# Optimization experiments

Measured on AMD Instinct MI355X. Metric: run time of the kernel, lower is better.

## Reference

```python
import jax, jax.numpy as jnp
import numpy as np

UNITS = 32      # 12 inter + 19 command + 1 motor
SENSORY = 32    # dense_2 output dim
MOTOR = 1
ODE_UNFOLDS = 6
EPS = 1e-8


def _build_wiring():
    # kerasncp NCP wiring: motor ids [0,1), command [1,20), inter [20,32)
    rng = np.random.RandomState(42)
    inter = np.arange(20, 32)
    command = np.arange(1, 20)
    motor = np.arange(0, 1)
    adj = np.zeros((UNITS, UNITS), np.float32)
    sens = np.zeros((SENSORY, UNITS), np.float32)
    for s in range(SENSORY):                      # sensory_fanout=6 onto inter neurons
        for d in rng.choice(inter, 6, replace=False):
            sens[s, d] = rng.choice([-1.0, 1.0])
    for i in inter:                               # inter_fanout=4 onto command neurons
        for d in rng.choice(command, 4, replace=False):
            adj[i, d] = rng.choice([-1.0, 1.0])
    for _ in range(6):                            # 6 recurrent command synapses
        adj[rng.choice(command), rng.choice(command)] = rng.choice([-1.0, 1.0])
    for m in motor:                               # motor_fanin=4 from command neurons
        for srcn in rng.choice(command, 4, replace=False):
            adj[srcn, m] = rng.choice([-1.0, 1.0])
    return adj, sens


def setup_inputs() -> dict:
    key = jax.random.key(0)
    ks = jax.random.split(key, 12)
    B, T = 256, 1024
    adj, sens = _build_wiring()
    u = lambda k, sh, lo, hi: jax.random.uniform(k, sh, jnp.float32, lo, hi)
    return {
        "x": jax.random.normal(ks[0], (B, T, 2), jnp.float32),
        "d1_w": jax.random.normal(ks[1], (2, 128), jnp.float32) * (1.0 / np.sqrt(2.0)),
        "d1_b": jnp.zeros((128,), jnp.float32),
        "d2_w": jax.random.normal(ks[2], (128, SENSORY), jnp.float32) * (1.0 / np.sqrt(128.0)),
        "d2_b": jnp.zeros((SENSORY,), jnp.float32),
        "input_w": jnp.ones((SENSORY,), jnp.float32),
        "input_b": jnp.zeros((SENSORY,), jnp.float32),
        "output_w": jnp.ones((MOTOR,), jnp.float32),
        "output_b": jnp.zeros((MOTOR,), jnp.float32),
        "gleak": u(ks[3], (UNITS,), 0.001, 1.0),
        "vleak": u(ks[4], (UNITS,), -0.2, 0.2),
        "cm": u(ks[5], (UNITS,), 0.4, 0.6),
        "w_syn": u(ks[6], (UNITS, UNITS), 0.001, 1.0),
        "mu": u(ks[7], (UNITS, UNITS), 0.3, 0.8),
        "sigma": u(ks[8], (UNITS, UNITS), 3.0, 8.0),
        "erev": jnp.asarray(adj),
        "sensory_w": u(ks[9], (SENSORY, UNITS), 0.001, 1.0),
        "sensory_mu": u(ks[10], (SENSORY, UNITS), 0.3, 0.8),
        "sensory_sigma": u(ks[11], (SENSORY, UNITS), 3.0, 8.0),
        "sensory_erev": jnp.asarray(sens),
        "sparsity_mask": jnp.asarray(np.abs(adj), jnp.int32),
        "sensory_mask": jnp.asarray(np.abs(sens), jnp.int32),
    }


def reference(x, d1_w, d1_b, d2_w, d2_b, input_w, input_b, output_w, output_b,
              gleak, vleak, cm, w_syn, mu, sigma, erev,
              sensory_w, sensory_mu, sensory_sigma, sensory_erev,
              sparsity_mask, sensory_mask):
    # Dense stack (per timestep)
    h = jax.nn.relu(x @ d1_w + d1_b)          # [B,T,128]
    h = h @ d2_w + d2_b                        # [B,T,32] sensory inputs
    spm = sparsity_mask.astype(h.dtype)
    ssm = sensory_mask.astype(h.dtype)

    def gate(v, m, s):                         # v [B,pre] -> [B,pre,post]
        return jax.nn.sigmoid(s * (v[..., None] - m))

    cm_t = cm * ODE_UNFOLDS                    # cm / (elapsed_time / ode_unfolds), elapsed_time=1

    def step(v, xt):
        inp = xt * input_w + input_b           # LTC input mapping (affine)
        sa = sensory_w * gate(inp, sensory_mu, sensory_sigma) * ssm   # [B,32,32]
        wnum_s = jnp.sum(sa * sensory_erev, axis=1)                   # [B,32]
        wden_s = jnp.sum(sa, axis=1)

        def unfold(vp, _):
            wa = w_syn * gate(vp, mu, sigma) * spm                    # [B,32,32]
            wnum = jnp.sum(wa * erev, axis=1) + wnum_s
            wden = jnp.sum(wa, axis=1) + wden_s
            vp = (cm_t * vp + gleak * vleak + wnum) / (cm_t + gleak + wden + EPS)
            return vp, None

        v, _ = jax.lax.scan(unfold, v, None, length=ODE_UNFOLDS)
        return v, None

    v0 = jnp.zeros((h.shape[0], UNITS), h.dtype)
    vT, _ = jax.lax.scan(step, v0, jnp.swapaxes(h, 0, 1))  # scan over T
    # output mapping: motor neurons are the first MOTOR states
    return vT[:, :MOTOR] * output_w + output_b             # [B,1]
```

## Files before the change

kernel.cpp:

```cpp
#include <hip/hip_runtime.h>
#include <math.h>

#define NB 256
#define NT 1024
#define NUNF 6
#define TBS 128
#define CHK 8
#define NTJMAX 12
#define L2E 1.44269504088896340736f
#define PI_F 3.14159265358979324f

typedef const float* fp;

extern "C" __device__ float __ocml_exp2_f32(float);
__device__ __forceinline__ float frcp(float x) { return __builtin_amdgcn_rcpf(x); }
__device__ __forceinline__ float ex2(float x) { return __ocml_exp2_f32(x); }
__device__ __forceinline__ float sgm(float a, float b, float v) { return frcp(1.f + ex2(fmaf(a, v, b))); }

struct Tables {
    int ngroups, npos, nchunks, ntraj;
    int grp_start[21];
    int ord[20];
    int pos[20];
    int aff[20];
    int need_traj[20];
    int traj_slot[20];
    int ch_ps[20], ch_pe[20], ch_gs[20], ch_ge[20];
    int ncp[20], nip[20], ngp[20];
    float cmt[20], cn0[20], cd0[20];
    float icmt[12];
    int   cp_pre[20][8];
    float cp_a[20][8], cp_b[20][8], cp_w[20][8], cp_e[20][8];
    int   ip_i[20][12];
    float ip_a[20][12], ip_b[20][12], ip_w[20][12], ip_e[20][12];
    int   gp_pre[20][6];
    float gp_a[20][6], gp_b[20][6], gp_w[20][6], gp_e[20][6];
};

struct DenseTab {
    int cnt[12];
    float in0[12], id0[12];
    int   pre[12][32];
    float a[12][32], b[12][32], w[12][32], e[12][32];
    int homog, maxcnt;
};

#define WS_DTAB   16384
#define WS_BND    24576
#define WS_BMASK  25600
#define WS_MG     32768
#define WS_VST    98304
#define WS_SENSI  131072

__global__ void build_tables(fp wsyn, fp mu, fp sigma, fp erev, const int* spm,
                             fp sw, fp smu, fp ssg, fp serev, const int* smask,
                             fp cm, fp gleak, fp vleak, fp d1b, Tables* T, DenseTab* D) {
    __shared__ int   spmL[1024], smkL[1024];
    __shared__ float wL[1024], muL[1024], sgL[1024], evL[1024];
    __shared__ float swL[1024], smuL[1024], ssgL[1024], sevL[1024];
    __shared__ float cmL[32], glL[32], vlL[32];
    __shared__ int premaskL[20], ancL[20], rootL[20], depUL[20], keyL[20], posL[20], ordL[20];
    __shared__ int ngpL[20], ntjL[20], slotU[20];
    __shared__ int neededS;
    __shared__ float habs[64];
    __shared__ int cntS[12];
    int tid = threadIdx.x;
    for (int k = tid; k < 1024; k += 64) {
        spmL[k] = spm[k]; wL[k] = wsyn[k]; muL[k] = mu[k]; sgL[k] = sigma[k]; evL[k] = erev[k];
        smkL[k] = smask[k]; swL[k] = sw[k]; smuL[k] = smu[k]; ssgL[k] = ssg[k]; sevL[k] = serev[k];
    }
    if (tid < 32) { cmL[tid] = cm[tid]; glL[tid] = gleak[tid]; vlL[tid] = vleak[tid]; }
    habs[tid] = fmaxf(fabsf(d1b[tid]), fabsf(d1b[tid + 64]));
    __syncthreads();
    if (tid < 20) {
        int pm = 0;
        for (int i = 0; i < 20; ++i) if (spmL[i * 32 + tid]) pm |= 1 << i;
        premaskL[tid] = pm;
        ancL[tid] = pm;
    }
    __syncthreads();
    for (int it = 0; it < 20; ++it) {
        int a = 0;
        if (tid < 20) {
            a = ancL[tid];
            int pm = premaskL[tid];
            for (int i = 0; i < 20; ++i) if ((pm >> i) & 1) a |= ancL[i];
        }
        __syncthreads();
        if (tid < 20) ancL[tid] = a;
        __syncthreads();
    }
    if (tid == 0) neededS = ancL[0] | 1;
    __syncthreads();
    int needed = neededS;
    if (tid < 20) {
        int r = tid;
        if ((needed >> tid) & 1) {
            int aj = ancL[tid];
            for (int i = 0; i < 20; ++i)
                if (i < r && ((needed >> i) & 1) && ((aj >> i) & 1) && ((ancL[i] >> tid) & 1)) r = i;
        }
        rootL[tid] = r;
        depUL[tid] = 0;
    }
    __syncthreads();
    for (int it = 0; it < 21; ++it) {
        int d = 0;
        if (tid < 20 && ((needed >> tid) & 1)) {
            int pm = premaskL[tid], myr = rootL[tid];
            for (int i = 0; i < 20; ++i)
                if (((pm >> i) & 1) && rootL[i] != myr) d = max(d, depUL[i] + 1);
        }
        __syncthreads();
        if (tid < 20 && d > depUL[tid]) depUL[tid] = d;
        __syncthreads();
    }
    if (tid < 20) {
        int key = 0x7FFFFFFF;
        if ((needed >> tid) & 1) {
            int myr = rootL[tid], dg = 0;
            for (int i = 0; i < 20; ++i)
                if (((needed >> i) & 1) && rootL[i] == myr) dg = max(dg, depUL[i]);
            key = dg * 32 + myr;
        }
        keyL[tid] = key;
    }
    __syncthreads();
    if (tid < 20) {
        int mykey = keyL[tid];
        int p = 0;
        for (int k = 0; k < 20; ++k)
            if (keyL[k] < mykey || (keyL[k] == mykey && k < tid)) ++p;
        posL[tid] = p;
        if (p < 20) ordL[p] = tid;
    }
    __syncthreads();
    if (tid < 20) {
        int nt = 0;
        if ((needed >> tid) & 1)
            for (int j = 0; j < 20; ++j)
                if (j != tid && ((needed >> j) & 1) && spmL[tid * 32 + j]) { nt = 1; break; }
        ntjL[tid] = nt;
    }
    __syncthreads();
    if (tid == 0) {
        int s = 0;
        for (int p = 0; p < 20; ++p) { int u = ordL[p]; slotU[u] = s; s += ntjL[u]; }
        T->ntraj = s;
    }
    __syncthreads();
    if (tid < 20) {
        int j = tid, cc = 0, ci = 0, cg = 0;
        T->cmt[j] = cmL[j] * (float)NUNF;
        T->cn0[j] = glL[j] * vlL[j];
        T->cd0[j] = cmL[j] * (float)NUNF + glL[j] + 1e-8f;
        if ((needed >> j) & 1) {
            int myr = rootL[j];
            int mystart = posL[myr];
            for (int i = 0; i < 32; ++i) {
                int p = i * 32 + j;
                if (!spmL[p]) continue;
                float sg = sgL[p];
                float a = -sg * L2E, b = sg * muL[p] * L2E;
                float w = wL[p], e = w * evL[p];
                if (i >= 20) {
                    T->ip_i[j][ci] = i - 20;
                    T->ip_a[j][ci] = a; T->ip_b[j][ci] = b; T->ip_w[j][ci] = w; T->ip_e[j][ci] = e;
                    ++ci;
                } else if (rootL[i] == myr) {
                    T->gp_pre[j][cg] = posL[i] - mystart;
                    T->gp_a[j][cg] = a; T->gp_b[j][cg] = b; T->gp_w[j][cg] = w; T->gp_e[j][cg] = e;
                    ++cg;
                } else {
                    T->cp_pre[j][cc] = slotU[i];
                    T->cp_a[j][cc] = a; T->cp_b[j][cc] = b; T->cp_w[j][cc] = w; T->cp_e[j][cc] = e;
                    ++cc;
                }
            }
        }
        T->ncp[j] = cc; T->nip[j] = ci; T->ngp[j] = cg;
        ngpL[j] = cg;
    }
    if (tid < 12) {
        T->icmt[tid] = cmL[20 + tid] * (float)NUNF;
        int unit = 20 + tid, cnt = 0;
        for (int s = 0; s < 32; ++s) {
            int p = s * 32 + unit;
            if (!smkL[p]) continue;
            float sg = ssgL[p];
            D->pre[tid][cnt] = s;
            D->a[tid][cnt] = -sg * L2E;
            D->b[tid][cnt] = sg * smuL[p] * L2E;
            D->w[tid][cnt] = swL[p];
            D->e[tid][cnt] = swL[p] * sevL[p];
            ++cnt;
        }
        for (int c = cnt; c < 32; ++c) {
            D->pre[tid][c] = 0; D->a[tid][c] = 0.f; D->b[tid][c] = 0.f;
            D->w[tid][c] = 0.f; D->e[tid][c] = 0.f;
        }
        D->cnt[tid] = cnt;
        cntS[tid] = cnt;
        D->in0[tid] = glL[unit] * vlL[unit];
        D->id0[tid] = cmL[unit] * (float)NUNF + glL[unit] + 1e-8f;
    }
    __syncthreads();
    if (tid == 0) {
        int npos = __popc(needed & 0xFFFFF);
        T->npos = npos;
        int ng = 0, prevkey = -1;
        for (int p = 0; p < npos; ++p) {
            int u = ordL[p];
            if (keyL[u] != prevkey) { T->grp_start[ng] = p; ++ng; prevkey = keyL[u]; }
        }
        T->ngroups = ng;
        for (int g = ng; g <= 20; ++g) T->grp_start[g] = npos;
        for (int p = 0; p < 20; ++p) T->ord[p] = (p < npos) ? ordL[p] : 0;
        for (int j = 0; j < 20; ++j) T->pos[j] = posL[j];
        for (int g = 0; g < ng; ++g) {
            int gs = T->grp_start[g], ge = T->grp_start[g + 1], gsz = ge - gs;
            for (int p = gs; p < ge; ++p)
                T->aff[p] = (gsz == 1 && ngpL[ordL[p]] == 0) ? 1 : 0;
        }
        for (int p = npos; p < 20; ++p) T->aff[p] = 0;
        for (int p = 0; p < 20; ++p) {
            int u = ordL[p];
            T->need_traj[p] = ntjL[u];
            T->traj_slot[p] = slotU[u];
        }
        int nchunks = 0, g = 0;
        while (g < ng) {
            int lvl = keyL[ordL[T->grp_start[g]]] / 32;
            int ge = g;
            while (ge < ng && keyL[ordL[T->grp_start[ge]]] / 32 == lvl) ++ge;
            int cs = g;
            while (cs < ge) {
                int ce = cs, acc = 0;
                while (ce < ge) {
                    int gsz = T->grp_start[ce + 1] - T->grp_start[ce];
                    if (acc + gsz > CHK && ce > cs) break;
                    acc += gsz; ++ce;
                    if (acc >= CHK) break;
                }
                T->ch_gs[nchunks] = cs; T->ch_ge[nchunks] = ce;
                T->ch_ps[nchunks] = T->grp_start[cs]; T->ch_pe[nchunks] = T->grp_start[ce];
                ++nchunks;
                cs = ce;
            }
            g = ge;
        }
        T->nchunks = nchunks;
        float hm = 0.f;
        for (int k = 0; k < 64; ++k) hm = fmaxf(hm, habs[k]);
        D->homog = (hm == 0.f) ? 1 : 0;
        int mc = 0;
        for (int k = 0; k < 12; ++k) mc = max(mc, cntS[k]);
        D->maxcnt = mc;
    }
}

__global__ void sector_prep(fp d1w, float* bnd, int* bmask) {
    __shared__ float ang[256];
    __shared__ float uS[128], vS[128];
    int tid = threadIdx.x;
    if (tid < 128) { uS[tid] = d1w[tid]; vS[tid] = d1w[128 + tid]; }
    __syncthreads();
    {
        int k = tid & 127;
        float al = atan2f(vS[k], uS[k]);
        float bb = (tid < 128) ? al + 1.57079632679489662f : al - 1.57079632679489662f;
        if (bb > PI_F) bb -= 2.f * PI_F;
        if (bb <= -PI_F) bb += 2.f * PI_F;
        ang[tid] = bb;
    }
    __syncthreads();
    for (int k = 2; k <= 256; k <<= 1) {
        for (int j = k >> 1; j > 0; j >>= 1) {
            int ixj = tid ^ j;
            if (ixj > tid) {
                float a0 = ang[tid], a1 = ang[ixj];
                bool up = ((tid & k) == 0);
                if ((a0 > a1) == up) { ang[tid] = a1; ang[ixj] = a0; }
            }
            __syncthreads();
        }
    }
    bnd[tid] = ang[tid];
    float lo = ang[tid];
    float hi = (tid < 255) ? ang[tid + 1] : ang[0] + 2.f * PI_F;
    float tm = 0.5f * (lo + hi);
    float ct = cosf(tm), st = sinf(tm);
    for (int w = 0; w < 4; ++w) {
        int m = 0;
        for (int kk = 0; kk < 32; ++kk) {
            int k = w * 32 + kk;
            if (fmaf(uS[k], ct, vS[k] * st) > 0.f) m |= 1 << kk;
        }
        bmask[tid * 4 + w] = m;
    }
}

__global__ void sector_M(fp d1w, fp d2w, fp iw, const int* bmask, float2* Mg) {
    int s = blockIdx.x, j = threadIdx.x;
    if (j >= 32) return;
    float acc0 = 0.f, acc1 = 0.f;
#pragma unroll
    for (int w = 0; w < 4; ++w) {
        int mm = bmask[s * 4 + w];
        for (int kk = 0; kk < 32; ++kk) {
            if ((mm >> kk) & 1) {
                int k = w * 32 + kk;
                float w2 = d2w[k * 32 + j];
                acc0 = fmaf(d1w[k], w2, acc0);
                acc1 = fmaf(d1w[128 + k], w2, acc1);
            }
        }
    }
    float iwj = iw[j];
    Mg[s * 32 + j] = make_float2(acc0 * iwj, acc1 * iwj);
}

__global__ __launch_bounds__(256) void dense_general(
    fp x, fp d1w, fp d1b, fp d2w, fp d2b, fp iw, fp ib,
    const DenseTab* __restrict__ Dg, float2* sensI, int t0, int CT) {
    if (Dg->homog != 0) return;
    __shared__ float W2s[4096];
    __shared__ float W1s[256], b1s[128];
    __shared__ float b2q[32], iwq[32], ibq[32];
    __shared__ float4 tabT[416];
    __shared__ int   preT[416];
    __shared__ int   cntL[12];
    __shared__ float in0L[12], id0L[12];
    __shared__ float hbuf[4][128][20];
    __shared__ float ibuf[4][16][33];
    int tid = threadIdx.x;
    for (int idx = tid; idx < 384; idx += 256) {
        int d = idx >> 5, e = idx & 31;
        int sl = e * 13 + d;
        tabT[sl] = make_float4(Dg->a[d][e], Dg->b[d][e], Dg->w[d][e], Dg->e[d][e]);
        preT[sl] = Dg->pre[d][e];
    }
    if (tid < 12) { cntL[tid] = Dg->cnt[tid]; in0L[tid] = Dg->in0[tid]; id0L[tid] = Dg->id0[tid]; }
    for (int p = tid; p < 4096; p += 256) W2s[p] = d2w[p];
    if (tid < 256) W1s[tid] = d1w[tid];
    if (tid < 128) b1s[tid] = d1b[tid];
    if (tid < 32) { b2q[tid] = d2b[tid]; iwq[tid] = iw[tid]; ibq[tid] = ib[tid]; }
    __syncthreads();
    int wid = tid >> 6, lane = tid & 63;
    float* hb = (float*)hbuf[wid];
    float* ibf = (float*)ibuf[wid];
    const float2* x2 = (const float2*)x;
    int gw = blockIdx.x * 4 + wid;
    int nw = gridDim.x * 4;
    int pass_total = (NB * CT) >> 4;
    int itd1 = lane >> 2, kq = lane & 3;
    int j = lane & 31, half = lane >> 5;
    for (int pass = gw; pass < pass_total; pass += nw) {
        int cg0 = pass * 16;
        {
            int cg = cg0 + itd1;
            int lt = cg >> 8, b = cg & 255;
            float2 xv = x2[b * NT + (t0 + lt)];
#pragma unroll 8
            for (int i = 0; i < 32; ++i) {
                int k = kq + 4 * i;
                float hk = fmaf(xv.y, W1s[128 + k], fmaf(xv.x, W1s[k], b1s[k]));
                hb[k * 20 + itd1] = hk > 0.f ? hk : 0.f;
            }
        }
        __builtin_amdgcn_wave_barrier();
        {
            float a0=0,a1=0,a2=0,a3=0,a4=0,a5=0,a6=0,a7=0;
#pragma unroll 4
            for (int k = 0; k < 128; ++k) {
                float w2 = W2s[k * 32 + j];
                float4 ha = *(const float4*)&hb[k * 20 + half * 8];
                float4 hbv = *(const float4*)&hb[k * 20 + half * 8 + 4];
                a0 = fmaf(ha.x, w2, a0); a1 = fmaf(ha.y, w2, a1);
                a2 = fmaf(ha.z, w2, a2); a3 = fmaf(ha.w, w2, a3);
                a4 = fmaf(hbv.x, w2, a4); a5 = fmaf(hbv.y, w2, a5);
                a6 = fmaf(hbv.z, w2, a6); a7 = fmaf(hbv.w, w2, a7);
            }
            float bb = b2q[j], iww = iwq[j], ibb = ibq[j];
            ibf[(half*8+0)*33+j] = fmaf(a0+bb, iww, ibb);
            ibf[(half*8+1)*33+j] = fmaf(a1+bb, iww, ibb);
            ibf[(half*8+2)*33+j] = fmaf(a2+bb, iww, ibb);
            ibf[(half*8+3)*33+j] = fmaf(a3+bb, iww, ibb);
            ibf[(half*8+4)*33+j] = fmaf(a4+bb, iww, ibb);
            ibf[(half*8+5)*33+j] = fmaf(a5+bb, iww, ibb);
            ibf[(half*8+6)*33+j] = fmaf(a6+bb, iww, ibb);
            ibf[(half*8+7)*33+j] = fmaf(a7+bb, iww, ibb);
        }
        __builtin_amdgcn_wave_barrier();
#pragma unroll
        for (int r = 0; r < 3; ++r) {
            int task = r * 64 + lane;
            int it = task / 12;
            int d = task - it * 12;
            int cnt = cntL[d];
            float wn = in0L[d], wd = id0L[d];
            for (int e = 0; e < cnt; ++e) {
                int sl = e * 13 + d;
                float4 tb = tabT[sl];
                float gq = frcp(1.f + ex2(fmaf(tb.x, ibf[it * 33 + preT[sl]], tb.y)));
                wn = fmaf(tb.w, gq, wn);
                wd = fmaf(tb.z, gq, wd);
            }
            int cg = cg0 + it;
            int lt = cg >> 8, b = cg & 255;
            sensI[(size_t)(b * CT + lt) * 12 + d] = make_float2(wn, wd);
        }
        __builtin_amdgcn_wave_barrier();
    }
}

__global__ __launch_bounds__(512) void solve(
    fp x, const float2* __restrict__ sensI,
    const Tables* __restrict__ Tg, const DenseTab* __restrict__ Dg,
    const float2* __restrict__ Mg, const float* __restrict__ bndg,
    fp d2b, fp iw, fp ib,
    fp ow, fp ob, float* vstate, int t0, int CT, float* out) {
    __shared__ Tables TL;
    __shared__ float2 iAB[TBS * 12];
    __shared__ float viter[TBS * 13];
    __shared__ float vtraj[NTJMAX * TBS * 7];
    __shared__ float2 pnpd[CHK * TBS * 7];
    __shared__ float2 comp[CHK * TBS];
    __shared__ float vstart[CHK * TBS];
    __shared__ float gstate[20], istate[12];
    __shared__ float bndL[256];
    __shared__ float4 tabT[416];
    __shared__ int   preT[416];
    __shared__ float b2qL[32], iwqL[32], ibqL[32];
    __shared__ float in0L[12], id0L[12];
    int tid = threadIdx.x;
    int b = blockIdx.x;
    {
        const int nw = (int)(sizeof(Tables) / 4);
        const int* src = (const int*)Tg;
        int* dst = (int*)&TL;
        for (int k = tid; k < nw; k += 512) dst[k] = src[k];
    }
    int homog = Dg->homog;
    int cntmax = Dg->maxcnt;
    if (homog) {
        for (int idx = tid; idx < 384; idx += 512) {
            int d = idx >> 5, e = idx & 31;
            int sl = e * 13 + d;
            tabT[sl] = make_float4(Dg->a[d][e], Dg->b[d][e], Dg->w[d][e], Dg->e[d][e]);
            preT[sl] = Dg->pre[d][e];
        }
        if (tid < 256) bndL[tid] = bndg[tid];
        if (tid < 32) { b2qL[tid] = d2b[tid]; iwqL[tid] = iw[tid]; ibqL[tid] = ib[tid]; }
        if (tid < 12) { in0L[tid] = Dg->in0[tid]; id0L[tid] = Dg->id0[tid]; }
    }
    __syncthreads();
    if (tid < 20 && tid < TL.npos)
        gstate[tid] = (t0 == 0) ? 0.f : vstate[b * 32 + TL.ord[tid]];
    if (tid < 12)
        istate[tid] = (t0 == 0) ? 0.f : vstate[b * 32 + 20 + tid];
    __syncthreads();
    int ntiles = CT / TBS;
    bool lastChunk = (t0 + CT == NT);
    const float2* x2 = (const float2*)x;
    for (int tile = 0; tile < ntiles; ++tile) {
        int tbase = tile * TBS;
        if (homog) {
            float* ibufL = (float*)pnpd;
            {
                int item = tid >> 2, q = tid & 3;
                float2 xv = x2[(size_t)b * NT + (t0 + tbase + item)];
                float th = atan2f(xv.y, xv.x);
                int sec;
                if (th < bndL[0]) sec = 255;
                else {
                    int lo = 0, hi = 255;
#pragma unroll
                    for (int it7 = 0; it7 < 8; ++it7) {
                        int mid = (lo + hi + 1) >> 1;
                        if (bndL[mid] <= th) lo = mid; else hi = mid - 1;
                    }
                    sec = lo;
                }
#pragma unroll
                for (int c = 0; c < 8; ++c) {
                    int j = q * 8 + c;
                    float2 m = Mg[sec * 32 + j];
                    float cj = fmaf(b2qL[j], iwqL[j], ibqL[j]);
                    ibufL[item * 33 + j] = fmaf(xv.x, m.x, fmaf(xv.y, m.y, cj));
                }
            }
            __syncthreads();
#pragma unroll
            for (int rb = 0; rb < 3; ++rb) {
                int task = rb * 512 + tid;
                int item = task / 12;
                int dd = task - item * 12;
                float wn = in0L[dd], wd = id0L[dd];
                for (int e = 0; e < cntmax; ++e) {
                    int sl = e * 13 + dd;
                    float4 tb = tabT[sl];
                    float gq = frcp(1.f + ex2(fmaf(tb.x, ibufL[item * 33 + preT[sl]], tb.y)));
                    wn = fmaf(tb.w, gq, wn);
                    wd = fmaf(tb.z, gq, wd);
                }
                float r = frcp(wd);
                iAB[item * 12 + dd] = make_float2(TL.icmt[dd] * r, wn * r);
            }
        } else {
            for (int w = tid; w < TBS * 16; w += 512) {
                int tt = w >> 4, ii = w & 15;
                if (ii < 12) {
                    float2 s = sensI[(size_t)(b * CT + tbase + tt) * 12 + ii];
                    float r = frcp(s.y);
                    iAB[tt * 12 + ii] = make_float2(TL.icmt[ii] * r, s.x * r);
                }
            }
        }
        __syncthreads();
        if (tid < 12) {
            float v = istate[tid];
#pragma unroll 4
            for (int tt = 0; tt < TBS; ++tt) {
                float2 ab = iAB[tt * 12 + tid];
                float A = ab.x, B = ab.y;
                float A2 = A * A, A4 = A2 * A2;
                float A6 = A4 * A2;
                float B6 = B * (1.f + A) * (1.f + A2 + A4);
                viter[tt * 13 + tid] = v;
                v = fmaf(A6, v, B6);
            }
            istate[tid] = v;
        }
        __syncthreads();
        int nchunks = TL.nchunks;
        for (int c = 0; c < nchunks; ++c) {
            int ps = TL.ch_ps[c], pe = TL.ch_pe[c];
            int gs0 = TL.ch_gs[c], ge0 = TL.ch_ge[c];
            int npc = pe - ps;
            for (int w = tid; w < npc * TBS; w += 512) {
                int m = w >> 7, tt = w & (TBS - 1);
                int posi = ps + m;
                int unit = TL.ord[posi];
                float pn[6], pd[6];
#pragma unroll
                for (int u = 0; u < 6; ++u) { pn[u] = TL.cn0[unit]; pd[u] = TL.cd0[unit]; }
                int ncp = TL.ncp[unit];
                for (int e = 0; e < ncp; ++e) {
                    int sl = TL.cp_pre[unit][e];
                    float a = TL.cp_a[unit][e], bb = TL.cp_b[unit][e];
                    float w_ = TL.cp_w[unit][e], ev = TL.cp_e[unit][e];
#pragma unroll
                    for (int u = 0; u < 6; ++u) {
                        float gq = sgm(a, bb, vtraj[(sl * TBS + tt) * 7 + u]);
                        pn[u] = fmaf(ev, gq, pn[u]);
                        pd[u] = fmaf(w_, gq, pd[u]);
                    }
                }
                int nip = TL.nip[unit];
                for (int e = 0; e < nip; ++e) {
                    int ii = TL.ip_i[unit][e];
                    float2 ab = iAB[tt * 12 + ii];
                    float vi = viter[tt * 13 + ii];
                    float a = TL.ip_a[unit][e], bb = TL.ip_b[unit][e];
                    float w_ = TL.ip_w[unit][e], ev = TL.ip_e[unit][e];
#pragma unroll
                    for (int u = 0; u < 6; ++u) {
                        float gq = sgm(a, bb, vi);
                        pn[u] = fmaf(ev, gq, pn[u]);
                        pd[u] = fmaf(w_, gq, pd[u]);
                        vi = fmaf(ab.x, vi, ab.y);
                    }
                }
                if (TL.aff[posi]) {
                    float cmt = TL.cmt[unit];
                    float Ac = 1.f, Bc = 0.f;
#pragma unroll
                    for (int u = 0; u < 6; ++u) {
                        float r = frcp(pd[u]);
                        float Au = cmt * r, Bu = pn[u] * r;
                        pnpd[(m * TBS + tt) * 7 + u] = make_float2(Au, Bu);
                        Bc = fmaf(Au, Bc, Bu);
                        Ac *= Au;
                    }
                    comp[m * TBS + tt] = make_float2(Ac, Bc);
                } else {
#pragma unroll
                    for (int u = 0; u < 6; ++u)
                        pnpd[(m * TBS + tt) * 7 + u] = make_float2(pn[u], pd[u]);
                }
            }
            __syncthreads();
            if (tid < ge0 - gs0) {
                int g = gs0 + tid;
                int gs = TL.grp_start[g], ge = TL.grp_start[g + 1], gsz = ge - gs;
                int m0 = gs - ps;
                if (gsz == 1) {
                    int unit = TL.ord[gs];
                    float v = gstate[gs];
                    if (TL.aff[gs]) {
#pragma unroll 4
                        for (int tt = 0; tt < TBS; ++tt) {
                            vstart[m0 * TBS + tt] = v;
                            float2 cc = comp[m0 * TBS + tt];
                            v = fmaf(cc.x, v, cc.y);
                        }
                    } else {
                        float ga = TL.gp_a[unit][0], gb = TL.gp_b[unit][0];
                        float gw = TL.gp_w[unit][0], gev = TL.gp_e[unit][0];
                        float cmt = TL.cmt[unit];
                        int ntj = TL.need_traj[gs];
                        int sl = TL.traj_slot[gs];
                        for (int tt = 0; tt < TBS; ++tt) {
#pragma unroll
                            for (int u = 0; u < 6; ++u) {
                                if (ntj) vtraj[(sl * TBS + tt) * 7 + u] = v;
                                float2 pp2 = pnpd[(m0 * TBS + tt) * 7 + u];
                                float E = ex2(fmaf(ga, v, gb));
                                float P = fmaf(cmt, v, pp2.x);
                                float N = fmaf(P, E, P + gev);
                                float Dd = fmaf(pp2.y, E, pp2.y + gw);
                                v = N * frcp(Dd);
                            }
                        }
                    }
                    gstate[gs] = v;
                } else {
                    float sv[CHK], nv[CHK];
#pragma unroll
                    for (int mm = 0; mm < CHK; ++mm) if (mm < gsz) sv[mm] = gstate[gs + mm];
                    for (int tt = 0; tt < TBS; ++tt) {
#pragma unroll
                        for (int u = 0; u < 6; ++u) {
#pragma unroll
                            for (int mm = 0; mm < CHK; ++mm)
                                if (mm < gsz && TL.need_traj[gs + mm])
                                    vtraj[(TL.traj_slot[gs + mm] * TBS + tt) * 7 + u] = sv[mm];
#pragma unroll
                            for (int mm = 0; mm < CHK; ++mm) {
                                if (mm < gsz) {
                                    int unit = TL.ord[gs + mm];
                                    float2 pp2 = pnpd[((m0 + mm) * TBS + tt) * 7 + u];
                                    float wn = pp2.x, wd = pp2.y;
                                    int ngpu = TL.ngp[unit];
#pragma unroll
                                    for (int e = 0; e < 6; ++e) {
                                        if (e < ngpu) {
                                            float vp = sv[TL.gp_pre[unit][e]];
                                            float gq = sgm(TL.gp_a[unit][e], TL.gp_b[unit][e], vp);
                                            wn = fmaf(TL.gp_e[unit][e], gq, wn);
                                            wd = fmaf(TL.gp_w[unit][e], gq, wd);
                                        }
                                    }
                                    nv[mm] = fmaf(TL.cmt[unit], sv[mm], wn) * frcp(wd);
                                }
                            }
#pragma unroll
                            for (int mm = 0; mm < CHK; ++mm) if (mm < gsz) sv[mm] = nv[mm];
                        }
                    }
#pragma unroll
                    for (int mm = 0; mm < CHK; ++mm) if (mm < gsz) gstate[gs + mm] = sv[mm];
                }
            }
            __syncthreads();
            for (int w = tid; w < npc * TBS; w += 512) {
                int m = w >> 7, tt = w & (TBS - 1);
                int posi = ps + m;
                if (TL.aff[posi] && TL.need_traj[posi]) {
                    int sl = TL.traj_slot[posi];
                    float v = vstart[m * TBS + tt];
#pragma unroll
                    for (int u = 0; u < 6; ++u) {
                        vtraj[(sl * TBS + tt) * 7 + u] = v;
                        float2 ab = pnpd[(m * TBS + tt) * 7 + u];
                        v = fmaf(ab.x, v, ab.y);
                    }
                }
            }
            __syncthreads();
        }
    }
    if (tid < 20 && tid < TL.npos) vstate[b * 32 + TL.ord[tid]] = gstate[tid];
    if (tid < 12) vstate[b * 32 + 20 + tid] = istate[tid];
    if (lastChunk) {
        __syncthreads();
        if (tid == 0) out[b] = fmaf(gstate[TL.pos[0]], ow[0], ob[0]);
    }
}

extern "C" void kernel_launch(void* const* d_in, const int* in_sizes, int n_in,
                              void* d_out, int out_size, void* d_ws, size_t ws_size,
                              hipStream_t stream) {
    fp x     = (fp)d_in[0];
    fp d1w   = (fp)d_in[1];
    fp d1b   = (fp)d_in[2];
    fp d2w   = (fp)d_in[3];
    fp d2b   = (fp)d_in[4];
    fp iw    = (fp)d_in[5];
    fp ib    = (fp)d_in[6];
    fp ow    = (fp)d_in[7];
    fp ob    = (fp)d_in[8];
    fp gleak = (fp)d_in[9];
    fp vleak = (fp)d_in[10];
    fp cm    = (fp)d_in[11];
    fp wsyn  = (fp)d_in[12];
    fp mu    = (fp)d_in[13];
    fp sigma = (fp)d_in[14];
    fp erev  = (fp)d_in[15];
    fp sw    = (fp)d_in[16];
    fp smu   = (fp)d_in[17];
    fp ssg   = (fp)d_in[18];
    fp serev = (fp)d_in[19];
    const int* spm   = (const int*)d_in[20];
    const int* smask = (const int*)d_in[21];

    char* wsb = (char*)d_ws;
    Tables*   T = (Tables*)wsb;
    DenseTab* D = (DenseTab*)(wsb + WS_DTAB);
    float*   bnd = (float*)(wsb + WS_BND);
    int*   bmask = (int*)(wsb + WS_BMASK);
    float2*   Mg = (float2*)(wsb + WS_MG);
    float* vstate = (float*)(wsb + WS_VST);
    float2* sensI = (float2*)(wsb + WS_SENSI);

    size_t per_t = (size_t)NB * 12 * sizeof(float2);
    int CT = TBS;
    if (ws_size > WS_SENSI) {
        size_t m = (ws_size - WS_SENSI) / per_t;
        int ct = TBS;
        while (ct < NT && (size_t)(ct * 2) <= m) ct *= 2;
        CT = ct;
    }

    build_tables<<<1, 64, 0, stream>>>(wsyn, mu, sigma, erev, spm,
                                       sw, smu, ssg, serev, smask,
                                       cm, gleak, vleak, d1b, T, D);
    sector_prep<<<1, 256, 0, stream>>>(d1w, bnd, bmask);
    sector_M<<<256, 64, 0, stream>>>(d1w, d2w, iw, bmask, Mg);

    int nch = NT / CT;
    for (int c = 0; c < nch; ++c) {
        int t0 = c * CT;
        dense_general<<<512, 256, 0, stream>>>(x, d1w, d1b, d2w, d2b, iw, ib, D, sensI, t0, CT);
        solve<<<NB, 512, 0, stream>>>(x, sensI, T, D, Mg, bnd, d2b, iw, ib,
                                      ow, ob, vstate, t0, CT, (float*)d_out);
    }
}
```

Before: 249.2 us.

## Double-buffer sensory input tables and compute next tile during serial chunk phase

Splits the per-tile sensory/interneuron coefficient buffer into two halves. The next tile's coefficients are computed by the otherwise idle threads (tid>=64) while the serial command-neuron chunk solve runs. Any leftover work is finished after the chunks. This removes the per-tile input stage and one barrier from the critical path, but each task now recomputes atan2 and the sector search per (item, dest) instead of once per item. CHK drops from 8 to 7 to shrink shared memory, and the input affine constant is precomputed into one table.

New measurement: 286.3 us. 1.15x slower.

```diff
diff --git a/kernel.cpp b/kernel.cpp
--- a/kernel.cpp
+++ b/kernel.cpp
@@ -5,7 +5,7 @@
 #define NT 1024
 #define NUNF 6
 #define TBS 128
-#define CHK 8
+#define CHK 7
 #define NTJMAX 12
 #define L2E 1.44269504088896340736f
 #define PI_F 3.14159265358979324f
@@ -421,7 +421,7 @@
     fp d2b, fp iw, fp ib,
     fp ow, fp ob, float* vstate, int t0, int CT, float* out) {
     __shared__ Tables TL;
-    __shared__ float2 iAB[TBS * 12];
+    __shared__ float2 iABb[2][TBS * 12];
     __shared__ float viter[TBS * 13];
     __shared__ float vtraj[NTJMAX * TBS * 7];
     __shared__ float2 pnpd[CHK * TBS * 7];
@@ -431,7 +431,7 @@
     __shared__ float bndL[256];
     __shared__ float4 tabT[416];
     __shared__ int   preT[416];
-    __shared__ float b2qL[32], iwqL[32], ibqL[32];
+    __shared__ float cjL[32];
     __shared__ float in0L[12], id0L[12];
     int tid = threadIdx.x;
     int b = blockIdx.x;
@@ -451,7 +451,7 @@
             preT[sl] = Dg->pre[d][e];
         }
         if (tid < 256) bndL[tid] = bndg[tid];
-        if (tid < 32) { b2qL[tid] = d2b[tid]; iwqL[tid] = iw[tid]; ibqL[tid] = ib[tid]; }
+        if (tid < 32) cjL[tid] = fmaf(d2b[tid], iw[tid], ib[tid]);
         if (tid < 12) { in0L[tid] = Dg->in0[tid]; id0L[tid] = Dg->id0[tid]; }
     }
     __syncthreads();
@@ -463,51 +463,58 @@
     int ntiles = CT / TBS;
     bool lastChunk = (t0 + CT == NT);
     const float2* x2 = (const float2*)x;
+    int nchunks = TL.nchunks;
+    if (homog) {
+        float* ibufL = (float*)pnpd;
+        {
+            int item = tid >> 2, q = tid & 3;
+            float2 xv = x2[(size_t)b * NT + (t0 + item)];
+            float th = atan2f(xv.y, xv.x);
+            int sec;
+            if (th < bndL[0]) sec = 255;
+            else {
+                int lo = 0, hi = 255;
+#pragma unroll
+                for (int it7 = 0; it7 < 8; ++it7) {
+                    int mid = (lo + hi + 1) >> 1;
+                    if (bndL[mid] <= th) lo = mid; else hi = mid - 1;
+                }
+                sec = lo;
+            }
+#pragma unroll
+            for (int c = 0; c < 8; ++c) {
+                int j = q * 8 + c;
+                float2 m = Mg[sec * 32 + j];
+                ibufL[item * 33 + j] = fmaf(xv.x, m.x, fmaf(xv.y, m.y, cjL[j]));
+            }
+        }
+        __syncthreads();
+#pragma unroll
+        for (int rb = 0; rb < 3; ++rb) {
+            int task = rb * 512 + tid;
+            int item = task / 12;
+            int dd = task - item * 12;
+            float wn = in0L[dd], wd = id0L[dd];
+            for (int e = 0; e < cntmax; ++e) {
+                int sl = e * 13 + dd;
+                float4 tb = tabT[sl];
+                float gq = frcp(1.f + ex2(fmaf(tb.x, ibufL[item * 33 + preT[sl]], tb.y)));
+                wn = fmaf(tb.w, gq, wn);
+                wd = fmaf(tb.z, gq, wd);
+            }
+            float r = frcp(wd);
+            iABb[0][item * 12 + dd] = make_float2(TL.icmt[dd] * r, wn * r);
+        }
+        __syncthreads();
+    }
     for (int tile = 0; tile < ntiles; ++tile) {
+        int cur = tile & 1;
         int tbase = tile * TBS;
-        if (homog) {
-            float* ibufL = (float*)pnpd;
-            {
-                int item = tid >> 2, q = tid & 3;
-                float2 xv = x2[(size_t)b * NT + (t0 + tbase + item)];
-                float th = atan2f(xv.y, xv.x);
-                int sec;
-                if (th < bndL[0]) sec = 255;
-                else {
-                    int lo = 0, hi = 255;
-#pragma unroll
-                    for (int it7 = 0; it7 < 8; ++it7) {
-                        int mid = (lo + hi + 1) >> 1;
-                        if (bndL[mid] <= th) lo = mid; else hi = mid - 1;
-                    }
-                    sec = lo;
-                }
-#pragma unroll
-                for (int c = 0; c < 8; ++c) {
-                    int j = q * 8 + c;
-                    float2 m = Mg[sec * 32 + j];
-                    float cj = fmaf(b2qL[j], iwqL[j], ibqL[j]);
-                    ibufL[item * 33 + j] = fmaf(xv.x, m.x, fmaf(xv.y, m.y, cj));
-                }
-            }
-            __syncthreads();
-#pragma unroll
-            for (int rb = 0; rb < 3; ++rb) {
-                int task = rb * 512 + tid;
-                int item = task / 12;
-                int dd = task - item * 12;
-                float wn = in0L[dd], wd = id0L[dd];
-                for (int e = 0; e < cntmax; ++e) {
-                    int sl = e * 13 + dd;
-                    float4 tb = tabT[sl];
-                    float gq = frcp(1.f + ex2(fmaf(tb.x, ibufL[item * 33 + preT[sl]], tb.y)));
-                    wn = fmaf(tb.w, gq, wn);
-                    wd = fmaf(tb.z, gq, wd);
-                }
-                float r = frcp(wd);
-                iAB[item * 12 + dd] = make_float2(TL.icmt[dd] * r, wn * r);
-            }
-        } else {
+        float2* iAB = iABb[cur];
+        float2* iABn = iABb[cur ^ 1];
+        bool mkNext = homog && (tile + 1 < ntiles);
+        int tnbase = t0 + (tile + 1) * TBS;
+        if (!homog) {
             for (int w = tid; w < TBS * 16; w += 512) {
                 int tt = w >> 4, ii = w & 15;
                 if (ii < 12) {
@@ -516,8 +523,8 @@
                     iAB[tt * 12 + ii] = make_float2(TL.icmt[ii] * r, s.x * r);
                 }
             }
-        }
-        __syncthreads();
+            __syncthreads();
+        }
         if (tid < 12) {
             float v = istate[tid];
 #pragma unroll 4
@@ -533,7 +540,6 @@
             istate[tid] = v;
         }
         __syncthreads();
-        int nchunks = TL.nchunks;
         for (int c = 0; c < nchunks; ++c) {
             int ps = TL.ch_ps[c], pe = TL.ch_pe[c];
             int gs0 = TL.ch_gs[c], ge0 = TL.ch_ge[c];
@@ -662,6 +668,37 @@
 #pragma unroll
                     for (int mm = 0; mm < CHK; ++mm) if (mm < gsz) gstate[gs + mm] = sv[mm];
                 }
+            } else if (mkNext && tid >= 64) {
+                for (int task = (tid - 64) + c * 448; task < 1536; task += nchunks * 448) {
+                    int item = task / 12;
+                    int dd = task - item * 12;
+                    float2 xv = x2[(size_t)b * NT + (tnbase + item)];
+                    float th = atan2f(xv.y, xv.x);
+                    int sec;
+                    if (th < bndL[0]) sec = 255;
+                    else {
+                        int lo = 0, hi = 255;
+#pragma unroll
+                        for (int it7 = 0; it7 < 8; ++it7) {
+                            int mid = (lo + hi + 1) >> 1;
+                            if (bndL[mid] <= th) lo = mid; else hi = mid - 1;
+                        }
+                        sec = lo;
+                    }
+                    float wn = in0L[dd], wd = id0L[dd];
+                    for (int e = 0; e < cntmax; ++e) {
+                        int sl = e * 13 + dd;
+                        float4 tb = tabT[sl];
+                        int pre = preT[sl];
+                        float2 m = Mg[sec * 32 + pre];
+                        float pv = fmaf(xv.x, m.x, fmaf(xv.y, m.y, cjL[pre]));
+                        float gq = frcp(1.f + ex2(fmaf(tb.x, pv, tb.y)));
+                        wn = fmaf(tb.w, gq, wn);
+                        wd = fmaf(tb.z, gq, wd);
+                    }
+                    float r = frcp(wd);
+                    iABn[item * 12 + dd] = make_float2(TL.icmt[dd] * r, wn * r);
+                }
             }
             __syncthreads();
             for (int w = tid; w < npc * TBS; w += 512) {
@@ -677,6 +714,39 @@
                         v = fmaf(ab.x, v, ab.y);
                     }
                 }
+            }
+            __syncthreads();
+        }
+        if (mkNext && nchunks * 448 < 1536) {
+            for (int task = nchunks * 448 + tid; task < 1536; task += 512) {
+                int item = task / 12;
+                int dd = task - item * 12;
+                float2 xv = x2[(size_t)b * NT + (tnbase + item)];
+                float th = atan2f(xv.y, xv.x);
+                int sec;
+                if (th < bndL[0]) sec = 255;
+                else {
+                    int lo = 0, hi = 255;
+#pragma unroll
+                    for (int it7 = 0; it7 < 8; ++it7) {
+                        int mid = (lo + hi + 1) >> 1;
+                        if (bndL[mid] <= th) lo = mid; else hi = mid - 1;
+                    }
+                    sec = lo;
+                }
+                float wn = in0L[dd], wd = id0L[dd];
+                for (int e = 0; e < cntmax; ++e) {
+                    int sl = e * 13 + dd;
+                    float4 tb = tabT[sl];
+                    int pre = preT[sl];
+                    float2 m = Mg[sec * 32 + pre];
+                    float pv = fmaf(xv.x, m.x, fmaf(xv.y, m.y, cjL[pre]));
+                    float gq = frcp(1.f + ex2(fmaf(tb.x, pv, tb.y)));
+                    wn = fmaf(tb.w, gq, wn);
+                    wd = fmaf(tb.z, gq, wd);
+                }
+                float r = frcp(wd);
+                iABn[item * 12 + dd] = make_float2(TL.icmt[dd] * r, wn * r);
             }
             __syncthreads();
         }
```

## Fuse sector kernels and dedupe per-item sector lookup in solve

Applied to the files above, without the earlier changes.

Merges the sector boundary/mask kernel and the per-sector matrix kernel into one single-block kernel that keeps masks and d2 weights in shared memory, removing a launch and a global round trip. In the solve kernel, the atan2 and binary search per time step are now done once per item by 128 threads and shared via LDS, rather than repeated by four threads each. The Mg gather is reorganised so lanes read contiguous columns, and the bias constant is precomputed. The fused sector kernel serialises a lot of work onto one block, which may lengthen setup.

New measurement: 531.3 us. +113.2%, slower.

```diff
diff --git a/kernel.cpp b/kernel.cpp
--- a/kernel.cpp
+++ b/kernel.cpp
@@ -47,7 +47,6 @@
 
 #define WS_DTAB   16384
 #define WS_BND    24576
-#define WS_BMASK  25600
 #define WS_MG     32768
 #define WS_VST    98304
 #define WS_SENSI  131072
@@ -259,11 +258,14 @@
     }
 }
 
-__global__ void sector_prep(fp d1w, float* bnd, int* bmask) {
+__global__ void sector_all(fp d1w, fp d2w, fp iw, float* bnd, float2* Mg) {
     __shared__ float ang[256];
     __shared__ float uS[128], vS[128];
+    __shared__ int bmaskL[256 * 4];
+    __shared__ float W2L[4096];
     int tid = threadIdx.x;
     if (tid < 128) { uS[tid] = d1w[tid]; vS[tid] = d1w[128 + tid]; }
+    for (int p = tid; p < 4096; p += 256) W2L[p] = d2w[p];
     __syncthreads();
     {
         int k = tid & 127;
@@ -296,28 +298,26 @@
             int k = w * 32 + kk;
             if (fmaf(uS[k], ct, vS[k] * st) > 0.f) m |= 1 << kk;
         }
-        bmask[tid * 4 + w] = m;
-    }
-}
-
-__global__ void sector_M(fp d1w, fp d2w, fp iw, const int* bmask, float2* Mg) {
-    int s = blockIdx.x, j = threadIdx.x;
-    if (j >= 32) return;
-    float acc0 = 0.f, acc1 = 0.f;
-#pragma unroll
-    for (int w = 0; w < 4; ++w) {
-        int mm = bmask[s * 4 + w];
-        for (int kk = 0; kk < 32; ++kk) {
-            if ((mm >> kk) & 1) {
-                int k = w * 32 + kk;
-                float w2 = d2w[k * 32 + j];
-                acc0 = fmaf(d1w[k], w2, acc0);
-                acc1 = fmaf(d1w[128 + k], w2, acc1);
-            }
-        }
-    }
-    float iwj = iw[j];
-    Mg[s * 32 + j] = make_float2(acc0 * iwj, acc1 * iwj);
+        bmaskL[tid * 4 + w] = m;
+    }
+    __syncthreads();
+    for (int j = 0; j < 32; ++j) {
+        float a0 = 0.f, a1 = 0.f;
+#pragma unroll
+        for (int w = 0; w < 4; ++w) {
+            int mm = bmaskL[tid * 4 + w];
+            for (int kk = 0; kk < 32; ++kk) {
+                if ((mm >> kk) & 1) {
+                    int k = w * 32 + kk;
+                    float w2 = W2L[k * 32 + j];
+                    a0 = fmaf(uS[k], w2, a0);
+                    a1 = fmaf(vS[k], w2, a1);
+                }
+            }
+        }
+        float iwj = iw[j];
+        Mg[tid * 32 + j] = make_float2(a0 * iwj, a1 * iwj);
+    }
 }
 
 __global__ __launch_bounds__(256) void dense_general(
@@ -431,8 +431,10 @@
     __shared__ float bndL[256];
     __shared__ float4 tabT[416];
     __shared__ int   preT[416];
-    __shared__ float b2qL[32], iwqL[32], ibqL[32];
+    __shared__ float cjL[32];
     __shared__ float in0L[12], id0L[12];
+    __shared__ int   secS[128];
+    __shared__ float x0S[128], x1S[128];
     int tid = threadIdx.x;
     int b = blockIdx.x;
     {
@@ -451,7 +453,7 @@
             preT[sl] = Dg->pre[d][e];
         }
         if (tid < 256) bndL[tid] = bndg[tid];
-        if (tid < 32) { b2qL[tid] = d2b[tid]; iwqL[tid] = iw[tid]; ibqL[tid] = ib[tid]; }
+        if (tid < 32) cjL[tid] = fmaf(d2b[tid], iw[tid], ib[tid]);
         if (tid < 12) { in0L[tid] = Dg->in0[tid]; id0L[tid] = Dg->id0[tid]; }
     }
     __syncthreads();
@@ -463,13 +465,13 @@
     int ntiles = CT / TBS;
     bool lastChunk = (t0 + CT == NT);
     const float2* x2 = (const float2*)x;
+    int nchunks = TL.nchunks;
     for (int tile = 0; tile < ntiles; ++tile) {
         int tbase = tile * TBS;
         if (homog) {
-            float* ibufL = (float*)pnpd;
-            {
-                int item = tid >> 2, q = tid & 3;
-                float2 xv = x2[(size_t)b * NT + (t0 + tbase + item)];
+            if (tid < 128) {
+                float2 xv = x2[(size_t)b * NT + (t0 + tbase + tid)];
+                x0S[tid] = xv.x; x1S[tid] = xv.y;
                 float th = atan2f(xv.y, xv.x);
                 int sec;
                 if (th < bndL[0]) sec = 255;
@@ -482,12 +484,18 @@
                     }
                     sec = lo;
                 }
+                secS[tid] = sec;
+            }
+            __syncthreads();
+            float* ibufL = (float*)pnpd;
+            {
+                int j = tid & 31, grp = tid >> 5;
+                float cj = cjL[j];
 #pragma unroll
                 for (int c = 0; c < 8; ++c) {
-                    int j = q * 8 + c;
-                    float2 m = Mg[sec * 32 + j];
-                    float cj = fmaf(b2qL[j], iwqL[j], ibqL[j]);
-                    ibufL[item * 33 + j] = fmaf(xv.x, m.x, fmaf(xv.y, m.y, cj));
+                    int item = grp * 8 + c;
+                    float2 m = Mg[secS[item] * 32 + j];
+                    ibufL[item * 33 + j] = fmaf(x0S[item], m.x, fmaf(x1S[item], m.y, cj));
                 }
             }
             __syncthreads();
@@ -533,7 +541,6 @@
             istate[tid] = v;
         }
         __syncthreads();
-        int nchunks = TL.nchunks;
         for (int c = 0; c < nchunks; ++c) {
             int ps = TL.ch_ps[c], pe = TL.ch_pe[c];
             int gs0 = TL.ch_gs[c], ge0 = TL.ch_ge[c];
@@ -719,7 +726,6 @@
     Tables*   T = (Tables*)wsb;
     DenseTab* D = (DenseTab*)(wsb + WS_DTAB);
     float*   bnd = (float*)(wsb + WS_BND);
-    int*   bmask = (int*)(wsb + WS_BMASK);
     float2*   Mg = (float2*)(wsb + WS_MG);
     float* vstate = (float*)(wsb + WS_VST);
     float2* sensI = (float2*)(wsb + WS_SENSI);
@@ -736,8 +742,7 @@
     build_tables<<<1, 64, 0, stream>>>(wsyn, mu, sigma, erev, spm,
                                        sw, smu, ssg, serev, smask,
                                        cm, gleak, vleak, d1b, T, D);
-    sector_prep<<<1, 256, 0, stream>>>(d1w, bnd, bmask);
-    sector_M<<<256, 64, 0, stream>>>(d1w, d2w, iw, bmask, Mg);
+    sector_all<<<1, 256, 0, stream>>>(d1w, d2w, iw, bnd, Mg);
 
     int nch = NT / CT;
     for (int c = 0; c < nch; ++c) {
```
